# Optimization experiments

Measured on AMD Instinct MI355X. Metric: run time of the kernel, lower is better.

Reference implementation:

```python
import jax, jax.numpy as jnp
import numpy as np
import math

HIDDEN = 1024
NUM_HEADS = 16
HEAD_DIM = HIDDEN // NUM_HEADS
B, S = 4, 1024


def setup_inputs() -> dict:
    key = jax.random.key(0)
    ks = jax.random.split(key, 16)
    sd = 1.0 / math.sqrt(HIDDEN)
    inp = {
        "x": jax.random.normal(ks[0], (B, S, HIDDEN), jnp.float32),
        "spikes": jax.random.uniform(ks[1], (B, S, HIDDEN), jnp.float32),
        "membrane_potential": jax.random.normal(ks[2], (B, S, HIDDEN), jnp.float32),
        "Wq": jax.random.normal(ks[3], (HIDDEN, HIDDEN), jnp.float32) * sd,
        "bq": jnp.zeros((HIDDEN,), jnp.float32),
        "Wk": jax.random.normal(ks[4], (HIDDEN, HIDDEN), jnp.float32) * sd,
        "bk": jnp.zeros((HIDDEN,), jnp.float32),
        "Wv": jax.random.normal(ks[5], (HIDDEN, HIDDEN), jnp.float32) * sd,
        "bv": jnp.zeros((HIDDEN,), jnp.float32),
        "Wo": jax.random.normal(ks[6], (HIDDEN, HIDDEN), jnp.float32) * sd,
        "bo": jnp.zeros((HIDDEN,), jnp.float32),
        "tau_decay": jnp.ones((NUM_HEADS,), jnp.float32) * 10.0,
        "Wg": jax.random.normal(ks[7], (HIDDEN, 2 * HIDDEN), jnp.float32) * sd,
        "bg": jnp.zeros((HIDDEN,), jnp.float32),
    }
    return inp


def _heads(t):  # [B,S,H] -> [B,nH,S,hd]
    Bv, Sv, _ = t.shape
    return t.reshape(Bv, Sv, NUM_HEADS, HEAD_DIM).transpose(0, 2, 1, 3)


def reference(x, spikes, membrane_potential, Wq, bq, Wk, bk, Wv, bv, Wo, bo, tau_decay, Wg, bg):
    scale = 1.0 / math.sqrt(HEAD_DIM)
    q = _heads(x @ Wq.T + bq)
    k = _heads(x @ Wk.T + bk)
    v = _heads(x @ Wv.T + bv)

    # raw scores [B,nH,S,S]
    scores = jnp.einsum('bhqd,bhkd->bhqk', q, k) * scale

    # per-head exponential temporal decay mask [nH,S,S]
    times = jnp.arange(S, dtype=jnp.float32)
    tdiff = jnp.abs(times[:, None] - times[None, :])  # [S,S]
    tmask = jnp.exp(-tdiff[None] / tau_decay[:, None, None])
    scores = scores * tmask[None]

    # spike correlation term
    sm = _heads(spikes)
    spike_attn = jnp.einsum('bhqd,bhkd->bhqk', sm, sm) * scale
    scores = scores * (1.0 + spike_attn)

    # membrane gating of V
    v = v * jax.nn.sigmoid(_heads(membrane_potential))

    probs = jax.nn.softmax(scores, axis=-1)
    context = jnp.einsum('bhqk,bhkd->bhqd', probs, v)
    context = context.transpose(0, 2, 1, 3).reshape(B, S, HIDDEN)

    # dendritic gate
    gate_in = jnp.concatenate([context, membrane_potential], axis=-1)
    gate = jax.nn.sigmoid(gate_in @ Wg.T + bg)
    context = context * gate

    return context @ Wo.T + bo
```

## Files before the change

### kernel.cpp

```cpp
#include <hip/hip_runtime.h>
#include <math.h>
#include <stdint.h>

namespace {

typedef __attribute__((ext_vector_type(8))) short s8v;
typedef __attribute__((ext_vector_type(4))) float f4v;
typedef unsigned short u16;

__device__ __forceinline__ float fexp2(float x) {
  return __builtin_amdgcn_exp2f(x);
}

__device__ __forceinline__ u16 f2bf(float f) {
  union { float f; uint32_t u; } v; v.f = f;
  uint32_t r = v.u + 0x7fffu + ((v.u >> 16) & 1u);
  return (u16)(r >> 16);
}
__device__ __forceinline__ float bf2f(u16 h) {
  union { uint32_t u; float f; } v; v.u = ((uint32_t)h) << 16;
  return v.f;
}
__device__ __forceinline__ uint32_t pk2r(float a, float b) {
  return (uint32_t)f2bf(a) | ((uint32_t)f2bf(b) << 16);
}
__device__ __forceinline__ uint32_t pk2(float a, float b) {
  union { float f; uint32_t u; } x, y; x.f = a; y.f = b;
  return ((x.u + 0x8000u) >> 16) | ((y.u + 0x8000u) & 0xffff0000u);
}
__device__ __forceinline__ float sigmoidf_(float x) { return 1.0f / (1.0f + __expf(-x)); }

__device__ __forceinline__ void gload16(const u16* g, u16* l) {
  __builtin_amdgcn_global_load_lds(
      (const __attribute__((address_space(1))) void*)g,
      (__attribute__((address_space(3))) void*)l, 16, 0, 0);
}

struct CvtJob { const float* src; u16* dst; };
struct CvtArgs { CvtJob j[18]; float* vz; };

__global__ __launch_bounds__(256) void cvt_kernel(CvtArgs a) {
  if (blockIdx.y == 0 && blockIdx.x < 4) {
    float4 z; z.x = 0.f; z.y = 0.f; z.z = 0.f; z.w = 0.f;
    ((float4*)a.vz)[blockIdx.x * 256 + threadIdx.x] = z;
  }
  const CvtJob jb = a.j[blockIdx.y];
  const int i = blockIdx.x * 256 + threadIdx.x;
  const float4 v = ((const float4*)jb.src)[i];
  uint2 pk;
  pk.x = pk2r(v.x, v.y);
  pk.y = pk2r(v.z, v.w);
  ((uint2*)jb.dst)[i] = pk;
}

__global__ __launch_bounds__(256) void qkv_gemm(
    const u16* __restrict__ xb,
    const u16* __restrict__ Wqb, const u16* __restrict__ Wkb, const u16* __restrict__ Wvb,
    const float* __restrict__ bq, const float* __restrict__ bk, const float* __restrict__ bv,
    const float* __restrict__ mem,
    u16* __restrict__ Qb, u16* __restrict__ Kb, u16* __restrict__ Vt,
    float* __restrict__ Vtot) {
  __shared__ u16 as_[8192], bs_[8192];
  const int t = threadIdx.x;
  const int nb = blockIdx.x, mb = blockIdx.y;
  const int sel = nb >> 3;
  const u16* W = sel == 0 ? Wqb : (sel == 1 ? Wkb : Wvb);
  const float* bias = sel == 0 ? bq : (sel == 1 ? bk : bv);
  const int m0 = mb * 128, n0 = (nb & 7) * 128;
  const f4v fz = {0.f, 0.f, 0.f, 0.f};
  f4v acc[4][4];
#pragma unroll
  for (int i = 0; i < 4; ++i)
#pragma unroll
    for (int j = 0; j < 4; ++j) acc[i][j] = fz;

  const int l = t & 63, w = t >> 6, wm = w >> 1, wn = w & 1;
  const int lr = l & 15, lq = l >> 4;
  const int rx = lr & 7;
  const int srow = t >> 3;
  const int scol = ((t & 7) ^ (srow & 7)) * 8;

#define QKV_STAGE(k0)                                                          \
  {                                                                            \
    const int kk_ = (k0);                                                      \
    _Pragma("unroll") for (int u = 0; u < 4; ++u) {                            \
      gload16(xb + (size_t)(m0 + u * 32 + srow) * 1024 + kk_ + scol,           \
              as_ + u * 2048 + t * 8);                                         \
      gload16(W + (size_t)(n0 + u * 32 + srow) * 1024 + kk_ + scol,            \
              bs_ + u * 2048 + t * 8);                                         \
    }                                                                          \
  }

  QKV_STAGE(0);

  if (sel < 2) {
    for (int c = 0; c < 16; ++c) {
      __syncthreads();
      s8v af[2][4], bf[2][4];
#pragma unroll
      for (int ks = 0; ks < 2; ++ks) {
        const int co = ((ks * 4 + lq) ^ rx) * 8;
#pragma unroll
        for (int mi = 0; mi < 4; ++mi)
          af[ks][mi] = *(const s8v*)(as_ + (wm * 64 + mi * 16 + lr) * 64 + co);
#pragma unroll
        for (int ni = 0; ni < 4; ++ni)
          bf[ks][ni] = *(const s8v*)(bs_ + (wn * 64 + ni * 16 + lr) * 64 + co);
      }
      __syncthreads();
      if (c < 15) QKV_STAGE((c + 1) << 6);
#pragma unroll
      for (int ks = 0; ks < 2; ++ks)
#pragma unroll
        for (int mi = 0; mi < 4; ++mi)
#pragma unroll
          for (int ni = 0; ni < 4; ++ni)
            acc[mi][ni] = __builtin_amdgcn_mfma_f32_16x16x32_bf16(
                bf[ks][ni], af[ks][mi], acc[mi][ni], 0, 0, 0);
    }
    u16* dst = (sel == 0) ? Qb : Kb;
#pragma unroll
    for (int mi = 0; mi < 4; ++mi)
#pragma unroll
      for (int ni = 0; ni < 4; ++ni) {
        const int m = m0 + wm * 64 + mi * 16 + lr;
        const int nb4 = n0 + wn * 64 + ni * 16 + lq * 4;
        const float4 b4 = *(const float4*)&bias[nb4];
        uint2 pk;
        pk.x = pk2r(acc[mi][ni][0] + b4.x, acc[mi][ni][1] + b4.y);
        pk.y = pk2r(acc[mi][ni][2] + b4.z, acc[mi][ni][3] + b4.w);
        *(uint2*)(dst + (size_t)m * 1024 + nb4) = pk;
      }
  } else {
    for (int c = 0; c < 16; ++c) {
      __syncthreads();
      s8v af[2][4], bf[2][4];
#pragma unroll
      for (int ks = 0; ks < 2; ++ks) {
        const int co = ((ks * 4 + lq) ^ rx) * 8;
#pragma unroll
        for (int mi = 0; mi < 4; ++mi)
          af[ks][mi] = *(const s8v*)(as_ + (wm * 64 + mi * 16 + lr) * 64 + co);
#pragma unroll
        for (int ni = 0; ni < 4; ++ni)
          bf[ks][ni] = *(const s8v*)(bs_ + (wn * 64 + ni * 16 + lr) * 64 + co);
      }
      __syncthreads();
      if (c < 15) QKV_STAGE((c + 1) << 6);
#pragma unroll
      for (int ks = 0; ks < 2; ++ks)
#pragma unroll
        for (int mi = 0; mi < 4; ++mi)
#pragma unroll
          for (int ni = 0; ni < 4; ++ni)
            acc[mi][ni] = __builtin_amdgcn_mfma_f32_16x16x32_bf16(
                af[ks][mi], bf[ks][ni], acc[mi][ni], 0, 0, 0);
    }
    const int b = m0 >> 10;
    float vpart[4] = {0.f, 0.f, 0.f, 0.f};
#pragma unroll
    for (int mi = 0; mi < 4; ++mi)
#pragma unroll
      for (int ni = 0; ni < 4; ++ni) {
        const int mrow = m0 + wm * 64 + mi * 16 + lq * 4;
        const int ncol = n0 + wn * 64 + ni * 16 + lr;
        const int h = ncol >> 6, d = ncol & 63;
        const float bi = bias[ncol];
        float tv[4];
#pragma unroll
        for (int r = 0; r < 4; ++r)
          tv[r] = (acc[mi][ni][r] + bi) * sigmoidf_(mem[(size_t)(mrow + r) * 1024 + ncol]);
        vpart[ni] += (tv[0] + tv[1]) + (tv[2] + tv[3]);
        const int s = mrow & 1023;
        uint2 pk;
        pk.x = pk2r(tv[0], tv[1]);
        pk.y = pk2r(tv[2], tv[3]);
        *(uint2*)(Vt + ((size_t)((b * 16 + h) * 64 + d)) * 1024 + s) = pk;
      }
#pragma unroll
    for (int ni = 0; ni < 4; ++ni) {
      const int ncol = n0 + wn * 64 + ni * 16 + lr;
      atomicAdd(&Vtot[(size_t)(b * 16 + (ncol >> 6)) * 64 + (ncol & 63)], vpart[ni]);
    }
  }
#undef QKV_STAGE
}

template <int MODE>
__global__ __launch_bounds__(256) void gemm64(
    const u16* __restrict__ Ab, const u16* __restrict__ A2b,
    const u16* __restrict__ W, const float* __restrict__ bias,
    u16* __restrict__ outb, float* __restrict__ outf, int K) {
  __shared__ u16 as_[8192], bs_[16384];
  const int t = threadIdx.x, l = t & 63, w = t >> 6;
  const int wm = w >> 1, wn = w & 1, lr = l & 15, lq = l >> 4;
  const int m0 = blockIdx.y * 64, n0 = blockIdx.x * 128;
  const f4v fz = {0.f, 0.f, 0.f, 0.f};
  f4v acc[2][4];
#pragma unroll
  for (int i = 0; i < 2; ++i)
#pragma unroll
    for (int j = 0; j < 4; ++j) acc[i][j] = fz;
  const int rx = lr & 7;
  const int srow = t >> 3;
  const int scol = ((t & 7) ^ (srow & 7)) * 8;
  const int nc = K >> 6;

#define G64_STAGE(k0, bsel)                                                    \
  {                                                                            \
    const int kk_ = (k0);                                                      \
    const u16* Ae_ = Ab;                                                       \
    int ka_ = kk_;                                                             \
    if (MODE == 1 && kk_ >= 1024) { Ae_ = A2b; ka_ = kk_ - 1024; }             \
    _Pragma("unroll") for (int u = 0; u < 2; ++u)                              \
        gload16(Ae_ + (size_t)(m0 + u * 32 + srow) * 1024 + ka_ + scol,        \
                as_ + (bsel) * 4096 + u * 2048 + t * 8);                       \
    _Pragma("unroll") for (int u = 0; u < 4; ++u)                              \
        gload16(W + (size_t)(n0 + u * 32 + srow) * K + kk_ + scol,             \
                bs_ + (bsel) * 8192 + u * 2048 + t * 8);                       \
  }

  G64_STAGE(0, 0);
  int pp = 0;
  for (int c = 0; c < nc; ++c) {
    __syncthreads();
    if (c + 1 < nc) G64_STAGE((c + 1) << 6, pp ^ 1);
    const int loA = pp * 4096, loB = pp * 8192;
#pragma unroll
    for (int ks = 0; ks < 2; ++ks) {
      const int co = ((ks * 4 + lq) ^ rx) * 8;
      s8v af[2], bf[4];
#pragma unroll
      for (int mi = 0; mi < 2; ++mi)
        af[mi] = *(const s8v*)(as_ + loA + (wm * 32 + mi * 16 + lr) * 64 + co);
#pragma unroll
      for (int ni = 0; ni < 4; ++ni)
        bf[ni] = *(const s8v*)(bs_ + loB + (wn * 64 + ni * 16 + lr) * 64 + co);
#pragma unroll
      for (int mi = 0; mi < 2; ++mi)
#pragma unroll
        for (int ni = 0; ni < 4; ++ni)
          acc[mi][ni] = __builtin_amdgcn_mfma_f32_16x16x32_bf16(
              bf[ni], af[mi], acc[mi][ni], 0, 0, 0);
    }
    pp ^= 1;
  }
#undef G64_STAGE

#pragma unroll
  for (int mi = 0; mi < 2; ++mi)
#pragma unroll
    for (int ni = 0; ni < 4; ++ni) {
      const int m = m0 + wm * 32 + mi * 16 + lr;
      const int nb4 = n0 + wn * 64 + ni * 16 + lq * 4;
      const float4 b4 = *(const float4*)&bias[nb4];
      if (MODE == 0) {
        float4 o;
        o.x = acc[mi][ni][0] + b4.x; o.y = acc[mi][ni][1] + b4.y;
        o.z = acc[mi][ni][2] + b4.z; o.w = acc[mi][ni][3] + b4.w;
        *(float4*)(outf + (size_t)m * 1024 + nb4) = o;
      } else {
        const uint2 a2 = *(const uint2*)(Ab + (size_t)m * 1024 + nb4);
        float cx[4] = {bf2f((u16)(a2.x & 0xffff)), bf2f((u16)(a2.x >> 16)),
                       bf2f((u16)(a2.y & 0xffff)), bf2f((u16)(a2.y >> 16))};
        float g[4];
        g[0] = cx[0] * sigmoidf_(acc[mi][ni][0] + b4.x);
        g[1] = cx[1] * sigmoidf_(acc[mi][ni][1] + b4.y);
        g[2] = cx[2] * sigmoidf_(acc[mi][ni][2] + b4.z);
        g[3] = cx[3] * sigmoidf_(acc[mi][ni][3] + b4.w);
        uint2 pk;
        pk.x = pk2r(g[0], g[1]);
        pk.y = pk2r(g[2], g[3]);
        *(uint2*)(outb + (size_t)m * 1024 + nb4) = pk;
      }
    }
}

__global__ __launch_bounds__(256) void attn_mfma(
    const u16* __restrict__ Qb, const u16* __restrict__ Kb,
    const u16* __restrict__ SPb, const u16* __restrict__ Vt,
    const float* __restrict__ tau, const float* __restrict__ Vtot,
    u16* __restrict__ CTXb) {
  __shared__ u16 kbuf[4096], skbuf[4096], vbuf[4096];
  __shared__ u16 pbuf[4][16 * 64];
  const int t = threadIdx.x, l = t & 63, w = t >> 6;
  const int lr = l & 15, lq = l >> 4;
  const int p = blockIdx.x;
  const int g = (p & 7) + 8 * (p >> 7);
  const int qt = (p >> 3) & 15;
  const int h = g & 15, b = g >> 4;

  const float tv_ = tau[h];
  const float c2 = 1.44269504088896f / tv_;
  const float K0 = 0.125f * 1.44269504088896f;
  int rad = (int)ceilf(tv_ * 0.171875f);
  if (rad > 15) rad = 15;
  const int jlo = (qt - rad < 0) ? 0 : qt - rad;
  const int jhi = (qt + rad > 15) ? 15 : qt + rad;
  const int farCnt = 16 - (jhi - jlo + 1);

  float cN[4], cNi[4], cR[4], cRi[4];
#pragma unroll
  for (int i = 0; i < 4; ++i) {
    cN[i]  = fexp2(c2 * (float)(i * 16));
    cNi[i] = fexp2(-c2 * (float)(i * 16));
    cR[i]  = fexp2(c2 * (float)(lq * 4 + i));
    cRi[i] = fexp2(-c2 * (float)(lq * 4 + i));
  }

  s8v qf[2], sf[2];
  {
    const size_t base = ((size_t)(b * 1024 + qt * 64 + w * 16 + lr)) * 1024 + h * 64 + lq * 8;
    qf[0] = *(const s8v*)(Qb + base);
    qf[1] = *(const s8v*)(Qb + base + 32);
    sf[0] = *(const s8v*)(SPb + base);
    sf[1] = *(const s8v*)(SPb + base + 32);
  }
  const s8v ones = {0x3F80, 0x3F80, 0x3F80, 0x3F80, 0x3F80, 0x3F80, 0x3F80, 0x3F80};

  const f4v fz = {0.f, 0.f, 0.f, 0.f};
  f4v oacc[4], vs[4];
  float lacc[4];
#pragma unroll
  for (int i = 0; i < 4; ++i) { oacc[i] = fz; vs[i] = fz; lacc[i] = 0.f; }

  const int iqw = qt * 64 + w * 16;
  const int srow = t >> 3;
  const int csw = ((t & 7) ^ (srow & 7)) * 8;
  const int rx = lr & 7;
  u16* pw = pbuf[w];

  for (int jc = jlo; jc <= jhi; ++jc) {
    const int j0 = jc * 64;
    __syncthreads();
    {
      const size_t kg = ((size_t)(b * 1024 + j0 + srow)) * 1024 + h * 64 + csw;
      gload16(Kb + kg, kbuf + t * 8);
      gload16(Kb + kg + 32 * 1024, kbuf + 2048 + t * 8);
      gload16(SPb + kg, skbuf + t * 8);
      gload16(SPb + kg + 32 * 1024, skbuf + 2048 + t * 8);
      const size_t vg = ((size_t)((b * 16 + h) * 64 + srow)) * 1024 + j0 + csw;
      gload16(Vt + vg, vbuf + t * 8);
      gload16(Vt + vg + 32 * 1024, vbuf + 2048 + t * 8);
    }
    __syncthreads();

    f4v sa[4], ssa[4];
#pragma unroll
    for (int ni = 0; ni < 4; ++ni) { sa[ni] = fz; ssa[ni] = fz; }
#pragma unroll
    for (int ks = 0; ks < 2; ++ks) {
#pragma unroll
      for (int ni = 0; ni < 4; ++ni) {
        const int off = (ni * 16 + lr) * 64 + (((ks * 4 + lq) ^ rx) * 8);
        const s8v kf = *(const s8v*)(kbuf + off);
        sa[ni] = __builtin_amdgcn_mfma_f32_16x16x32_bf16(kf, qf[ks], sa[ni], 0, 0, 0);
        const s8v skf = *(const s8v*)(skbuf + off);
        ssa[ni] = __builtin_amdgcn_mfma_f32_16x16x32_bf16(skf, sf[ks], ssa[ni], 0, 0, 0);
      }
    }

    const int D0 = iqw - j0;
    float pv[4][4];
    if (jc < qt) {
      const float EA = K0 * fexp2(-c2 * (float)(D0 + lr));
#pragma unroll
      for (int ni = 0; ni < 4; ++ni)
#pragma unroll
        for (int r = 0; r < 4; ++r) {
          const float t1 = fmaf(ssa[ni][r], 0.125f, 1.0f);
          const float e = fexp2(sa[ni][r] * cN[ni] * cR[r] * EA * t1);
          pv[ni][r] = e;
          lacc[ni] += e;
        }
    } else if (jc > qt) {
      const float EAi = K0 * fexp2(c2 * (float)(D0 + lr));
#pragma unroll
      for (int ni = 0; ni < 4; ++ni)
#pragma unroll
        for (int r = 0; r < 4; ++r) {
          const float t1 = fmaf(ssa[ni][r], 0.125f, 1.0f);
          const float e = fexp2(sa[ni][r] * cNi[ni] * cRi[r] * EAi * t1);
          pv[ni][r] = e;
          lacc[ni] += e;
        }
    } else {
      const float EA  = K0 * fexp2(-c2 * (float)(D0 + lr));
      const float EAi = K0 * fexp2(c2 * (float)(D0 + lr));
#pragma unroll
      for (int ni = 0; ni < 4; ++ni)
#pragma unroll
        for (int r = 0; r < 4; ++r) {
          const int jloc = ni * 16 + lq * 4 + r;
          const float fb = cN[ni] * cR[r] * EA;
          const float fa = cNi[ni] * cRi[r] * EAi;
          const float f = (D0 + lr >= jloc) ? fb : fa;
          const float t1 = fmaf(ssa[ni][r], 0.125f, 1.0f);
          const float e = fexp2(sa[ni][r] * f * t1);
          pv[ni][r] = e;
          lacc[ni] += e;
        }
    }

#pragma unroll
    for (int ni = 0; ni < 4; ++ni) {
      const int phys = (ni * 2 + (lq >> 1)) ^ rx;
      uint2 p2;
      p2.x = pk2(pv[ni][0], pv[ni][1]);
      p2.y = pk2(pv[ni][2], pv[ni][3]);
      *(uint2*)(pw + lr * 64 + phys * 8 + (lq & 1) * 4) = p2;
    }

#pragma unroll
    for (int ks = 0; ks < 2; ++ks) {
      const s8v pf = *(const s8v*)(pw + lr * 64 + (((ks * 4 + lq) ^ rx) * 8));
#pragma unroll
      for (int nd = 0; nd < 4; ++nd) {
        const int off = (nd * 16 + lr) * 64 + (((ks * 4 + lq) ^ rx) * 8);
        const s8v vf = *(const s8v*)(vbuf + off);
        oacc[nd] = __builtin_amdgcn_mfma_f32_16x16x32_bf16(vf, pf, oacc[nd], 0, 0, 0);
        vs[nd] = __builtin_amdgcn_mfma_f32_16x16x32_bf16(vf, ones, vs[nd], 0, 0, 0);
      }
    }
  }

  float ls = (lacc[0] + lacc[1]) + (lacc[2] + lacc[3]);
  ls += __shfl_xor(ls, 16);
  ls += __shfl_xor(ls, 32);
  ls += 64.0f * (float)farCnt;
  const float inv = 1.0f / ls;
  const float* vt0 = Vtot + (size_t)(b * 16 + h) * 64;
  const size_t orow = ((size_t)(b * 1024 + qt * 64 + w * 16 + lr)) * 1024 + h * 64;
#pragma unroll
  for (int nd = 0; nd < 4; ++nd) {
    const float4 vt4 = *(const float4*)(vt0 + nd * 16 + lq * 4);
    float o0 = (oacc[nd][0] + vt4.x - vs[nd][0]) * inv;
    float o1 = (oacc[nd][1] + vt4.y - vs[nd][1]) * inv;
    float o2 = (oacc[nd][2] + vt4.z - vs[nd][2]) * inv;
    float o3 = (oacc[nd][3] + vt4.w - vs[nd][3]) * inv;
    uint2 o;
    o.x = pk2r(o0, o1);
    o.y = pk2r(o2, o3);
    *(uint2*)(CTXb + orow + nd * 16 + lq * 4) = o;
  }
}

}

extern "C" void kernel_launch(void* const* d_in, const int* in_sizes, int n_in,
                              void* d_out, int out_size, void* d_ws, size_t ws_size,
                              hipStream_t stream) {
  const float* x      = (const float*)d_in[0];
  const float* spikes = (const float*)d_in[1];
  const float* mem    = (const float*)d_in[2];
  const float* Wq     = (const float*)d_in[3];
  const float* bq     = (const float*)d_in[4];
  const float* Wk     = (const float*)d_in[5];
  const float* bk     = (const float*)d_in[6];
  const float* Wv     = (const float*)d_in[7];
  const float* bv     = (const float*)d_in[8];
  const float* Wo     = (const float*)d_in[9];
  const float* bo     = (const float*)d_in[10];
  const float* tau    = (const float*)d_in[11];
  const float* Wg     = (const float*)d_in[12];
  const float* bg     = (const float*)d_in[13];
  float* out = (float*)d_out;

  uint8_t* w8 = (uint8_t*)d_ws;
  u16* spb  = (u16*)(w8);
  u16* xb   = (u16*)(w8 + (8u << 20));
  u16* Wqb  = (u16*)(w8 + (16u << 20));
  u16* Wkb  = (u16*)(w8 + (18u << 20));
  u16* Wvb  = (u16*)(w8 + (20u << 20));
  u16* Wob  = (u16*)(w8 + (22u << 20));
  u16* Wgb  = (u16*)(w8 + (24u << 20));
  u16* Qb   = (u16*)(w8 + (28u << 20));
  u16* Kb   = (u16*)(w8 + (36u << 20));
  u16* Vt   = (u16*)(w8 + (44u << 20));
  u16* CTXb = (u16*)(w8 + (52u << 20));
  float* Vtot = (float*)(w8 + (60u << 20));
  u16* memb = (u16*)d_out;
  u16* gctx = xb;

  constexpr size_t QE = 262144 * 4;
  CvtArgs ca;
  for (int q = 0; q < 4; ++q) ca.j[q]     = {x + q * QE,      xb + q * QE};
  for (int q = 0; q < 4; ++q) ca.j[4 + q] = {spikes + q * QE, spb + q * QE};
  for (int q = 0; q < 4; ++q) ca.j[8 + q] = {mem + q * QE,    memb + q * QE};
  ca.j[12] = {Wq, Wqb};
  ca.j[13] = {Wk, Wkb};
  ca.j[14] = {Wv, Wvb};
  ca.j[15] = {Wo, Wob};
  ca.j[16] = {Wg, Wgb};
  ca.j[17] = {Wg + QE, Wgb + QE};
  ca.vz = Vtot;
  cvt_kernel<<<dim3(1024, 18), 256, 0, stream>>>(ca);

  qkv_gemm<<<dim3(24, 32), 256, 0, stream>>>(xb, Wqb, Wkb, Wvb, bq, bk, bv, mem,
                                             Qb, Kb, Vt, Vtot);
  attn_mfma<<<dim3(1024), 256, 0, stream>>>(Qb, Kb, spb, Vt, tau, Vtot, CTXb);
  gemm64<1><<<dim3(8, 64), 256, 0, stream>>>(CTXb, memb, Wgb, bg, gctx, nullptr, 2048);
  gemm64<0><<<dim3(8, 64), 256, 0, stream>>>(gctx, nullptr, Wob, bo, nullptr, out, 1024);
}
```

Baseline: 257.0 us.

## Pipeline QKV and gemm64 loads two stages deep with explicit waitcnt barriers

The QKV GEMM moves from a single-buffered 64-wide K stage to a double-buffered 32-wide K stage with a new swizzled LDS layout. Global loads for stage c+2 are issued while computing stage c, and each step syncs with explicit vmcnt/lgkmcnt waits and raw s_barrier instead of __syncthreads. gemm64 gets the same prefetch-two-ahead pipeline, plus s_setprio around the MFMA block in both kernels. The aim is to hide global-load latency behind MFMA work. The cost is more fragile hand-tuned synchronization, and the narrower K step doubles the number of barriers in QKV.

```diff
diff --git a/kernel.cpp b/kernel.cpp
--- a/kernel.cpp
+++ b/kernel.cpp
@@ -60,7 +60,7 @@
     const float* __restrict__ mem,
     u16* __restrict__ Qb, u16* __restrict__ Kb, u16* __restrict__ Vt,
     float* __restrict__ Vtot) {
-  __shared__ u16 as_[8192], bs_[8192];
+  __shared__ __align__(16) u16 as_[2][4096], bs_[2][4096];
   const int t = threadIdx.x;
   const int nb = blockIdx.x, mb = blockIdx.y;
   const int sel = nb >> 3;
@@ -76,48 +76,61 @@
 
   const int l = t & 63, w = t >> 6, wm = w >> 1, wn = w & 1;
   const int lr = l & 15, lq = l >> 4;
-  const int rx = lr & 7;
-  const int srow = t >> 3;
-  const int scol = ((t & 7) ^ (srow & 7)) * 8;
-
-#define QKV_STAGE(k0)                                                          \
+  const int rh = lr >> 1;
+  const int rb4 = (lr & 1) << 2;
+
+  const int sc0 = (t & 7) ^ ((t >> 3) & 7);
+  const int sgrow = ((t >> 3) << 1) + (sc0 >> 2);
+  const int sgk = (sc0 & 3) << 3;
+
+#define QKV_STAGE(k0, bsel)                                                    \
   {                                                                            \
     const int kk_ = (k0);                                                      \
-    _Pragma("unroll") for (int u = 0; u < 4; ++u) {                            \
-      gload16(xb + (size_t)(m0 + u * 32 + srow) * 1024 + kk_ + scol,           \
-              as_ + u * 2048 + t * 8);                                         \
-      gload16(W + (size_t)(n0 + u * 32 + srow) * 1024 + kk_ + scol,            \
-              bs_ + u * 2048 + t * 8);                                         \
+    _Pragma("unroll") for (int u = 0; u < 2; ++u) {                            \
+      gload16(xb + (size_t)(m0 + u * 64 + sgrow) * 1024 + kk_ + sgk,           \
+              &as_[bsel][u * 2048 + t * 8]);                                   \
+      gload16(W + (size_t)(n0 + u * 64 + sgrow) * 1024 + kk_ + sgk,            \
+              &bs_[bsel][u * 2048 + t * 8]);                                   \
     }                                                                          \
   }
 
-  QKV_STAGE(0);
+  QKV_STAGE(0, 0);
+  QKV_STAGE(32, 1);
+  asm volatile("s_waitcnt vmcnt(4)" ::: "memory");
+  __builtin_amdgcn_s_barrier();
 
   if (sel < 2) {
-    for (int c = 0; c < 16; ++c) {
-      __syncthreads();
-      s8v af[2][4], bf[2][4];
-#pragma unroll
-      for (int ks = 0; ks < 2; ++ks) {
-        const int co = ((ks * 4 + lq) ^ rx) * 8;
-#pragma unroll
-        for (int mi = 0; mi < 4; ++mi)
-          af[ks][mi] = *(const s8v*)(as_ + (wm * 64 + mi * 16 + lr) * 64 + co);
+    for (int c = 0; c < 32; ++c) {
+      const int pp = c & 1;
+      s8v af[4], bf[4];
+#pragma unroll
+      for (int mi = 0; mi < 4; ++mi)
+        af[mi] = *(const s8v*)(&as_[pp][(wm * 32 + mi * 8 + rh) * 64 +
+                                        (((rb4 + lq) ^ rh) * 8)]);
+#pragma unroll
+      for (int ni = 0; ni < 4; ++ni)
+        bf[ni] = *(const s8v*)(&bs_[pp][(wn * 32 + ni * 8 + rh) * 64 +
+                                        (((rb4 + lq) ^ rh) * 8)]);
+      asm volatile("s_waitcnt lgkmcnt(0)" ::: "memory");
+      __builtin_amdgcn_sched_barrier(0);
+      __builtin_amdgcn_s_barrier();
+      if (c + 2 < 32) QKV_STAGE((c + 2) << 5, pp);
+      __builtin_amdgcn_s_setprio(1);
+#pragma unroll
+      for (int mi = 0; mi < 4; ++mi)
 #pragma unroll
         for (int ni = 0; ni < 4; ++ni)
-          bf[ks][ni] = *(const s8v*)(bs_ + (wn * 64 + ni * 16 + lr) * 64 + co);
-      }
-      __syncthreads();
-      if (c < 15) QKV_STAGE((c + 1) << 6);
-#pragma unroll
-      for (int ks = 0; ks < 2; ++ks)
-#pragma unroll
-        for (int mi = 0; mi < 4; ++mi)
-#pragma unroll
-          for (int ni = 0; ni < 4; ++ni)
-            acc[mi][ni] = __builtin_amdgcn_mfma_f32_16x16x32_bf16(
-                bf[ks][ni], af[ks][mi], acc[mi][ni], 0, 0, 0);
-    }
+          acc[mi][ni] = __builtin_amdgcn_mfma_f32_16x16x32_bf16(
+              bf[ni], af[mi], acc[mi][ni], 0, 0, 0);
+      __builtin_amdgcn_s_setprio(0);
+      if (c + 2 < 32) {
+        asm volatile("s_waitcnt vmcnt(4)" ::: "memory");
+      } else if (c + 1 < 32) {
+        asm volatile("s_waitcnt vmcnt(0)" ::: "memory");
+      }
+      if (c + 1 < 32) __builtin_amdgcn_s_barrier();
+    }
+    __builtin_amdgcn_sched_barrier(0);
     u16* dst = (sel == 0) ? Qb : Kb;
 #pragma unroll
     for (int mi = 0; mi < 4; ++mi)
@@ -132,30 +145,37 @@
         *(uint2*)(dst + (size_t)m * 1024 + nb4) = pk;
       }
   } else {
-    for (int c = 0; c < 16; ++c) {
-      __syncthreads();
-      s8v af[2][4], bf[2][4];
-#pragma unroll
-      for (int ks = 0; ks < 2; ++ks) {
-        const int co = ((ks * 4 + lq) ^ rx) * 8;
-#pragma unroll
-        for (int mi = 0; mi < 4; ++mi)
-          af[ks][mi] = *(const s8v*)(as_ + (wm * 64 + mi * 16 + lr) * 64 + co);
+    for (int c = 0; c < 32; ++c) {
+      const int pp = c & 1;
+      s8v af[4], bf[4];
+#pragma unroll
+      for (int mi = 0; mi < 4; ++mi)
+        af[mi] = *(const s8v*)(&as_[pp][(wm * 32 + mi * 8 + rh) * 64 +
+                                        (((rb4 + lq) ^ rh) * 8)]);
+#pragma unroll
+      for (int ni = 0; ni < 4; ++ni)
+        bf[ni] = *(const s8v*)(&bs_[pp][(wn * 32 + ni * 8 + rh) * 64 +
+                                        (((rb4 + lq) ^ rh) * 8)]);
+      asm volatile("s_waitcnt lgkmcnt(0)" ::: "memory");
+      __builtin_amdgcn_sched_barrier(0);
+      __builtin_amdgcn_s_barrier();
+      if (c + 2 < 32) QKV_STAGE((c + 2) << 5, pp);
+      __builtin_amdgcn_s_setprio(1);
+#pragma unroll
+      for (int mi = 0; mi < 4; ++mi)
 #pragma unroll
         for (int ni = 0; ni < 4; ++ni)
-          bf[ks][ni] = *(const s8v*)(bs_ + (wn * 64 + ni * 16 + lr) * 64 + co);
-      }
-      __syncthreads();
-      if (c < 15) QKV_STAGE((c + 1) << 6);
-#pragma unroll
-      for (int ks = 0; ks < 2; ++ks)
-#pragma unroll
-        for (int mi = 0; mi < 4; ++mi)
-#pragma unroll
-          for (int ni = 0; ni < 4; ++ni)
-            acc[mi][ni] = __builtin_amdgcn_mfma_f32_16x16x32_bf16(
-                af[ks][mi], bf[ks][ni], acc[mi][ni], 0, 0, 0);
-    }
+          acc[mi][ni] = __builtin_amdgcn_mfma_f32_16x16x32_bf16(
+              af[mi], bf[ni], acc[mi][ni], 0, 0, 0);
+      __builtin_amdgcn_s_setprio(0);
+      if (c + 2 < 32) {
+        asm volatile("s_waitcnt vmcnt(4)" ::: "memory");
+      } else if (c + 1 < 32) {
+        asm volatile("s_waitcnt vmcnt(0)" ::: "memory");
+      }
+      if (c + 1 < 32) __builtin_amdgcn_s_barrier();
+    }
+    __builtin_amdgcn_sched_barrier(0);
     const int b = m0 >> 10;
     float vpart[4] = {0.f, 0.f, 0.f, 0.f};
 #pragma unroll
@@ -191,7 +211,7 @@
     const u16* __restrict__ Ab, const u16* __restrict__ A2b,
     const u16* __restrict__ W, const float* __restrict__ bias,
     u16* __restrict__ outb, float* __restrict__ outf, int K) {
-  __shared__ u16 as_[8192], bs_[16384];
+  __shared__ __align__(16) u16 as_[8192], bs_[16384];
   const int t = threadIdx.x, l = t & 63, w = t >> 6;
   const int wm = w >> 1, wn = w & 1, lr = l & 15, lq = l >> 4;
   const int m0 = blockIdx.y * 64, n0 = blockIdx.x * 128;
@@ -221,30 +241,46 @@
   }
 
   G64_STAGE(0, 0);
-  int pp = 0;
+  G64_STAGE(64, 1);
+  asm volatile("s_waitcnt vmcnt(6)" ::: "memory");
+  __builtin_amdgcn_s_barrier();
+
   for (int c = 0; c < nc; ++c) {
-    __syncthreads();
-    if (c + 1 < nc) G64_STAGE((c + 1) << 6, pp ^ 1);
+    const int pp = c & 1;
     const int loA = pp * 4096, loB = pp * 8192;
+    s8v af[2][2], bf[2][4];
 #pragma unroll
     for (int ks = 0; ks < 2; ++ks) {
       const int co = ((ks * 4 + lq) ^ rx) * 8;
-      s8v af[2], bf[4];
 #pragma unroll
       for (int mi = 0; mi < 2; ++mi)
-        af[mi] = *(const s8v*)(as_ + loA + (wm * 32 + mi * 16 + lr) * 64 + co);
+        af[ks][mi] = *(const s8v*)(as_ + loA + (wm * 32 + mi * 16 + lr) * 64 + co);
 #pragma unroll
       for (int ni = 0; ni < 4; ++ni)
-        bf[ni] = *(const s8v*)(bs_ + loB + (wn * 64 + ni * 16 + lr) * 64 + co);
+        bf[ks][ni] = *(const s8v*)(bs_ + loB + (wn * 64 + ni * 16 + lr) * 64 + co);
+    }
+    asm volatile("s_waitcnt lgkmcnt(0)" ::: "memory");
+    __builtin_amdgcn_sched_barrier(0);
+    __builtin_amdgcn_s_barrier();
+    if (c + 2 < nc) G64_STAGE((c + 2) << 6, pp);
+    __builtin_amdgcn_s_setprio(1);
+#pragma unroll
+    for (int ks = 0; ks < 2; ++ks)
 #pragma unroll
       for (int mi = 0; mi < 2; ++mi)
 #pragma unroll
         for (int ni = 0; ni < 4; ++ni)
           acc[mi][ni] = __builtin_amdgcn_mfma_f32_16x16x32_bf16(
-              bf[ni], af[mi], acc[mi][ni], 0, 0, 0);
-    }
-    pp ^= 1;
-  }
+              bf[ks][ni], af[ks][mi], acc[mi][ni], 0, 0, 0);
+    __builtin_amdgcn_s_setprio(0);
+    if (c + 2 < nc) {
+      asm volatile("s_waitcnt vmcnt(6)" ::: "memory");
+    } else if (c + 1 < nc) {
+      asm volatile("s_waitcnt vmcnt(0)" ::: "memory");
+    }
+    if (c + 1 < nc) __builtin_amdgcn_s_barrier();
+  }
+  __builtin_amdgcn_sched_barrier(0);
 #undef G64_STAGE
 
 #pragma unroll
```

New measurement: 255.7 us. No clear change (-0.5%).
